# Kernel optimization log

Hardware: AMD Instinct MI355X
Metric: run time of the kernel (lower is better)

## Reference

```python
import jax, jax.numpy as jnp
import numpy as np

B, N, D, H = 8, 1024, 1024, 16
HEAD_DIM = D // H
SCALING = HEAD_DIM ** (-0.5)
NEG = -1000000000.0


def setup_inputs() -> dict:
    key = jax.random.key(0)
    ks = jax.random.split(key, 7)
    x = jax.random.normal(ks[0], (B, N, D), dtype=jnp.float32)
    # variable-length batch: lengths in [N//2, N], mask[b, i] = i < len_b
    lengths = jax.random.randint(ks[1], (B,), N // 2, N + 1)
    mask = jnp.arange(N)[None, :] < lengths[:, None]  # [B, N] bool
    s = D ** (-0.5)
    Wk = jax.random.normal(ks[2], (D, D), dtype=jnp.float32) * s
    Wq = jax.random.normal(ks[3], (D, D), dtype=jnp.float32) * s
    Wv = jax.random.normal(ks[4], (D, D), dtype=jnp.float32) * s
    Wo = jax.random.normal(ks[5], (D, D), dtype=jnp.float32) * s
    bo = jnp.zeros((D,), dtype=jnp.float32)
    return {"x": x, "mask": mask, "Wk": Wk, "Wq": Wq, "Wv": Wv, "Wo": Wo, "bo": bo}


def reference(x, mask, Wk, Wq, Wv, Wo, bo):
    # torch nn.Linear: y = x @ W.T
    keys = (x @ Wk.T).reshape(B, N, H, HEAD_DIM)
    queries = (x @ Wq.T).reshape(B, N, H, HEAD_DIM)
    values = (x @ Wv.T).reshape(B, N, H, HEAD_DIM)
    # NOTE: faithful to source: keys on i, queries on j, softmax over j
    scores = jnp.einsum('bihx,bjhx->bhij', keys, queries) * SCALING  # [B,H,N,N]
    pair_mask = mask[:, None, :] & mask[:, :, None]                  # [B,N,N]
    scores = scores + jnp.where(pair_mask, 0.0, NEG)[:, None, :, :]
    attn = jax.nn.softmax(scores, axis=-1)
    out = jnp.einsum('bhij,bjhx->bihx', attn, values)                # [B,N,H,hd]
    out = out.reshape(B, N, D)
    out = out @ Wo.T + bo
    # source does out_dense[mask] (ragged); static-shape equivalent: zero padding
    return out * mask[:, :, None].astype(out.dtype)
```

## Files before the change

### kernel.cpp

```cpp
#include <hip/hip_runtime.h>

typedef unsigned short u16;
typedef __attribute__((ext_vector_type(8))) short short8;
typedef __attribute__((ext_vector_type(4))) short short4v;
typedef __attribute__((ext_vector_type(4))) float f32x4;
typedef __attribute__((ext_vector_type(16))) float f32x16;

#define MFMA16(a, b, c) __builtin_amdgcn_mfma_f32_16x16x32_bf16(a, b, c, 0, 0, 0)
#define MFMA32(a, b, c) __builtin_amdgcn_mfma_f32_32x32x16_bf16(a, b, c, 0, 0, 0)

#define BB 8
#define NN 1024
#define DD 1024
#define HH 16
#define HD 64
#define MM (BB * NN)
#define SCLOG2 0.18033688011112042f

static __device__ __forceinline__ u16 f2bf(float f) {
  unsigned u = __float_as_uint(f);
  u += 0x7fffu + ((u >> 16) & 1u);
  return (u16)(u >> 16);
}

static __device__ __forceinline__ void gld16(const void* g, void* l) {
  __builtin_amdgcn_global_load_lds((const __attribute__((address_space(1))) void*)g,
                                   (__attribute__((address_space(3))) void*)l, 16, 0, 0);
}

static __device__ __forceinline__ unsigned cvtpk(float lo, float hi) {
  unsigned r;
  asm("v_cvt_pk_bf16_f32 %0, %1, %2" : "=v"(r) : "v"(lo), "v"(hi));
  return r;
}

static __device__ __forceinline__ f32x16 zero16() {
  f32x16 v;
#pragma unroll
  for (int i = 0; i < 16; ++i) v[i] = 0.f;
  return v;
}

__global__ __launch_bounds__(256) void cast_bf16_kernel(const float* __restrict__ in,
                                                        u16* __restrict__ out, int n8) {
  const int i = blockIdx.x * 256 + threadIdx.x;
  if (i >= n8) return;
  const f32x4* p = (const f32x4*)in + (size_t)i * 2;
  const f32x4 a = p[0], b = p[1];
  short8 o;
  o[0] = (short)f2bf(a[0]); o[1] = (short)f2bf(a[1]);
  o[2] = (short)f2bf(a[2]); o[3] = (short)f2bf(a[3]);
  o[4] = (short)f2bf(b[0]); o[5] = (short)f2bf(b[1]);
  o[6] = (short)f2bf(b[2]); o[7] = (short)f2bf(b[3]);
  *(short8*)(out + (size_t)i * 8) = o;
}

__global__ __launch_bounds__(256) void cast4_lens_kernel(const float* __restrict__ a, const float* __restrict__ b,
                                                         const float* __restrict__ c, const float* __restrict__ d,
                                                         u16* __restrict__ oa, u16* __restrict__ ob,
                                                         u16* __restrict__ oc, u16* __restrict__ od,
                                                         const unsigned char* __restrict__ mask,
                                                         int* __restrict__ lens) {
  if (blockIdx.y == 4) {
    if (blockIdx.x != 0) return;
    __shared__ int acc[BB];
    const int t = threadIdx.x;
    if (t < BB) acc[t] = 0;
    __syncthreads();
    const bool isbyte = (mask[1] != 0);
    for (int bb = 0; bb < BB; ++bb) {
      int s = 0;
      if (isbyte) {
        for (int i = t; i < NN; i += 256) s += mask[(size_t)bb * NN + i] ? 1 : 0;
      } else {
        const int* mi = (const int*)mask;
        for (int i = t; i < NN; i += 256) s += mi[(size_t)bb * NN + i] != 0 ? 1 : 0;
      }
      if (s) atomicAdd(&acc[bb], s);
    }
    __syncthreads();
    if (t < BB) lens[t] = acc[t];
    return;
  }
  const int i = blockIdx.x * 256 + threadIdx.x;
  const float* in;
  u16* out;
  switch (blockIdx.y) {
    case 0: in = a; out = oa; break;
    case 1: in = b; out = ob; break;
    case 2: in = c; out = oc; break;
    default: in = d; out = od; break;
  }
  const f32x4* p = (const f32x4*)in + (size_t)i * 2;
  const f32x4 va = p[0], vb = p[1];
  short8 o;
  o[0] = (short)f2bf(va[0]); o[1] = (short)f2bf(va[1]);
  o[2] = (short)f2bf(va[2]); o[3] = (short)f2bf(va[3]);
  o[4] = (short)f2bf(vb[0]); o[5] = (short)f2bf(vb[1]);
  o[6] = (short)f2bf(vb[2]); o[7] = (short)f2bf(vb[3]);
  *(short8*)(out + (size_t)i * 8) = o;
}

#define STAGE_G(d, k0_)                                                            \
  _Pragma("unroll") for (int p = 0; p < 2; ++p) {                                  \
    const int off = (p * 256 + t) * 16;                                            \
    const int row = off >> 6;                                                      \
    const int colb = (off & 63) ^ (((row >> 1) & 3) << 4);                         \
    gld16(Ag + (size_t)(m0 + row) * 1024 + (k0_) + (colb >> 1), &As[d][off >> 1]); \
    gld16(Bg + (size_t)(n0 + row) * 1024 + (k0_) + (colb >> 1), &Bs[d][off >> 1]); \
  }

#define GEMM_CORE2()                                                            \
  STAGE_G(0, 0)                                                                 \
  __syncthreads();                                                              \
  for (int k0 = 0; k0 < 1024; k0 += 32) {                                       \
    const int cur = (k0 >> 5) & 1;                                              \
    if (k0 + 32 < 1024) { STAGE_G(cur ^ 1, k0 + 32) }                           \
    short8 af[4], bf[4];                                                        \
    _Pragma("unroll") for (int mi = 0; mi < 4; ++mi) {                          \
      const int row = wr * 64 + mi * 16 + li;                                   \
      const int byo = row * 64 + ((lg * 16) ^ (((row >> 1) & 3) << 4));         \
      af[mi] = *(const short8*)((const char*)&As[cur][0] + byo);                \
    }                                                                           \
    _Pragma("unroll") for (int ni = 0; ni < 4; ++ni) {                          \
      const int row = wc * 64 + ni * 16 + li;                                   \
      const int byo = row * 64 + ((lg * 16) ^ (((row >> 1) & 3) << 4));         \
      bf[ni] = *(const short8*)((const char*)&Bs[cur][0] + byo);                \
    }                                                                           \
    __builtin_amdgcn_s_setprio(1);                                              \
    _Pragma("unroll") for (int mi = 0; mi < 4; ++mi)                            \
      _Pragma("unroll") for (int ni = 0; ni < 4; ++ni)                          \
          acc[mi][ni] = MFMA16(af[mi], bf[ni], acc[mi][ni]);                    \
    __builtin_amdgcn_s_setprio(0);                                              \
    __syncthreads();                                                            \
  }

__global__ __launch_bounds__(256) void gemm_qkv(const u16* __restrict__ A,
                                                const u16* __restrict__ Wk3, const u16* __restrict__ Wq3,
                                                const u16* __restrict__ Wv3,
                                                u16* __restrict__ kb, u16* __restrict__ qb,
                                                u16* __restrict__ vtb, const int* __restrict__ lens) {
  const int m0 = blockIdx.x * 128;
  if ((m0 & 1023) >= lens[m0 >> 10]) return;
  __shared__ u16 As[2][4096];
  __shared__ u16 Bs[2][4096];
  const int mat = blockIdx.y >> 3;
  const int n0 = (blockIdx.y & 7) * 128;
  const u16* Ag = A;
  const u16* Bg = (mat == 0) ? Wk3 : (mat == 1) ? Wq3 : Wv3;
  const int t = threadIdx.x;
  const int lane = t & 63;
  const int w = t >> 6;
  const int wr = w >> 1, wc = w & 1;
  const int li = lane & 15, lg = lane >> 4;
  f32x4 acc[4][4] = {};

  GEMM_CORE2()

  if (mat == 2) {
#pragma unroll
    for (int mi = 0; mi < 4; ++mi) {
      const int row = m0 + wr * 64 + mi * 16 + lg * 4;
      const int bb = row >> 10, jj = row & 1023;
#pragma unroll
      for (int ni = 0; ni < 4; ++ni) {
        const int col = n0 + wc * 64 + ni * 16 + li;
        const int h = col >> 6, x = col & 63;
        short4v st;
#pragma unroll
        for (int r = 0; r < 4; ++r) st[r] = (short)f2bf(acc[mi][ni][r]);
        *(short4v*)(vtb + ((size_t)((bb * HH + h) * HD + x)) * NN + jj) = st;
      }
    }
  } else {
    u16* C = (mat == 0) ? kb : qb;
    const float scale = (mat == 0) ? SCLOG2 : 1.0f;
#pragma unroll
    for (int mi = 0; mi < 4; ++mi)
#pragma unroll
      for (int ni = 0; ni < 4; ++ni) {
        const int col = n0 + wc * 64 + ni * 16 + li;
        const int rowb = m0 + wr * 64 + mi * 16 + lg * 4;
#pragma unroll
        for (int r = 0; r < 4; ++r)
          C[(size_t)(rowb + r) * 1024 + col] = f2bf(acc[mi][ni][r] * scale);
      }
  }
}

__global__ __launch_bounds__(256) void gemm_out(const u16* __restrict__ A, const u16* __restrict__ Bw,
                                                float* __restrict__ C, const float* __restrict__ bias,
                                                const int* __restrict__ lens) {
  const int m0 = blockIdx.x * 128;
  const int n0 = blockIdx.y * 128;
  const int t = threadIdx.x;
  if ((m0 & 1023) >= lens[m0 >> 10]) {
    const int r = t >> 1, ch = (t & 1) * 64;
    float* Crow = C + (size_t)(m0 + r) * 1024 + n0 + ch;
    const f32x4 z = {0.f, 0.f, 0.f, 0.f};
#pragma unroll
    for (int c = 0; c < 16; ++c) *(f32x4*)(Crow + c * 4) = z;
    return;
  }
  __shared__ u16 As[2][4096];
  __shared__ u16 Bs[2][4096];
  const u16* Ag = A;
  const u16* Bg = Bw;
  const int lane = t & 63;
  const int w = t >> 6;
  const int wr = w >> 1, wc = w & 1;
  const int li = lane & 15, lg = lane >> 4;
  f32x4 acc[4][4] = {};

  GEMM_CORE2()

#pragma unroll
  for (int ni = 0; ni < 4; ++ni) {
    const int col = n0 + wc * 64 + ni * 16 + li;
    const float bv = bias[col];
#pragma unroll
    for (int mi = 0; mi < 4; ++mi) {
      const int rowb = m0 + wr * 64 + mi * 16 + lg * 4;
#pragma unroll
      for (int r = 0; r < 4; ++r) {
        const int row = rowb + r;
        const int bb = row >> 10, ii = row & 1023;
        const float v = (ii < lens[bb]) ? (acc[mi][ni][r] + bv) : 0.f;
        C[(size_t)row * 1024 + col] = v;
      }
    }
  }
}

#define QK_PART(JC, SN0_, SN1_)                                                \
  { const u16* Qc = &Qs[(JC) & 1][0];                                          \
    SN0_ = zero16(); SN1_ = zero16();                                          \
    __builtin_amdgcn_s_setprio(1);                                             \
    _Pragma("unroll") for (int ks = 0; ks < 4; ++ks) {                         \
      const short8 qf = *(const short8*)(Qc + (ks * 64 + l) * 8);              \
      SN0_ = MFMA32(qf, kf[ks], SN0_); }                                       \
    _Pragma("unroll") for (int ks = 0; ks < 4; ++ks) {                         \
      const short8 qf = *(const short8*)(Qc + ((4 + ks) * 64 + l) * 8);        \
      SN1_ = MFMA32(qf, kf[ks], SN1_); }                                       \
    __builtin_amdgcn_s_setprio(0); }

#define V_READ(JC, VF_)                                                        \
  { const u16* Vc = &Vs[(JC) & 1][0];                                          \
    _Pragma("unroll") for (int kk = 0; kk < 8; ++kk)                           \
      VF_[kk] = *(const short8*)(Vc + (kk * 64 + l) * 8); }

#define SM_PV(S0_, S1_, VF_)                                                   \
  {                                                                            \
    float pmax = S0_[0];                                                       \
    _Pragma("unroll") for (int r = 1; r < 16; ++r) pmax = fmaxf(pmax, S0_[r]); \
    _Pragma("unroll") for (int r = 0; r < 16; ++r) pmax = fmaxf(pmax, S1_[r]); \
    pmax = fmaxf(pmax, __shfl_xor(pmax, 32));                                  \
    if (!__all(pmax <= m_run + 11.5f)) {                    \
      const float mnew = fmaxf(m_run, pmax);                                   \
      const float al = __builtin_amdgcn_exp2f(m_run - mnew);                   \
      l_run *= al;                                                             \
      _Pragma("unroll") for (int r = 0; r < 16; ++r) { o0[r] *= al; o1[r] *= al; } \
      m_run = mnew;                                                            \
    }                                                                          \
    float rs = 0.f;                                                            \
    _Pragma("unroll") for (int r = 0; r < 16; ++r) {                           \
      const float p = __builtin_amdgcn_exp2f(S0_[r] - m_run); S0_[r] = p; rs += p; } \
    _Pragma("unroll") for (int r = 0; r < 16; ++r) {                           \
      const float p = __builtin_amdgcn_exp2f(S1_[r] - m_run); S1_[r] = p; rs += p; } \
    rs += __shfl_xor(rs, 32);                                                  \
    l_run += rs;                                                               \
                     \
    short8 pf[4];                                                              \
    _Pragma("unroll") for (int jk = 0; jk < 4; ++jk) {                         \
      const f32x16& ss = (jk < 2) ? S0_ : S1_;                                 \
      const int kk2 = jk & 1;                                                  \
      unsigned W0 = cvtpk(ss[8 * kk2 + 0], ss[8 * kk2 + 1]);                   \
      unsigned W1 = cvtpk(ss[8 * kk2 + 2], ss[8 * kk2 + 3]);                   \
      unsigned W2 = cvtpk(ss[8 * kk2 + 4], ss[8 * kk2 + 5]);                   \
      unsigned W3 = cvtpk(ss[8 * kk2 + 6], ss[8 * kk2 + 7]);                   \
      asm("v_permlane32_swap_b32 %0, %1" : "+v"(W0), "+v"(W2));                \
      asm("v_permlane32_swap_b32 %0, %1" : "+v"(W1), "+v"(W3));                \
      union { unsigned u[4]; short8 s; } pu;                                   \
      pu.u[0] = W0; pu.u[1] = W1; pu.u[2] = W2; pu.u[3] = W3;                  \
      pf[jk] = pu.s;                                                           \
    }                                                                          \
    __builtin_amdgcn_s_setprio(1);                                             \
    _Pragma("unroll") for (int kg = 0; kg < 4; ++kg) o0 = MFMA32(VF_[kg], pf[kg], o0); \
    _Pragma("unroll") for (int kg = 0; kg < 4; ++kg) o1 = MFMA32(VF_[4 + kg], pf[kg], o1); \
    __builtin_amdgcn_s_setprio(0);                                             \
  }

#define MASK_LAST(S0_, S1_)                                                    \
  { const int j0m = (nt - 1) * 64;                                             \
    if (j0m + 64 > len) {                                                      \
      _Pragma("unroll") for (int r = 0; r < 16; ++r) {                         \
        const int jl = (r & 3) + 8 * (r >> 2) + 4 * hi;                        \
        if (j0m + jl >= len) S0_[r] = -3.0e38f;                                \
        if (j0m + 32 + jl >= len) S1_[r] = -3.0e38f;                           \
      } } }

#define ATTN_BODY(JT, SP0, SP1, VFP, SN0, SN1, VFN)                            \
  { const int jc = (JT);                                                       \
    if (jc + 1 < nt) STAGE((jc + 1) & 1, (jc + 1) * 64);                       \
    QK_PART(jc, SN0, SN1)                                                      \
    SM_PV(SP0, SP1, VFP)                                                       \
    V_READ(jc, VFN)                                                            \
    __syncthreads(); }

__global__ __launch_bounds__(256) void attn_kernel(const u16* __restrict__ Kb, const u16* __restrict__ Qb,
                                                   const u16* __restrict__ Vtb, u16* __restrict__ attb,
                                                   const int* __restrict__ lens) {
  const int bid = blockIdx.x;
  const int b = bid >> 7;
  const int ic = (bid >> 3) & 7;
  const int h = ((bid & 7) << 1) | ((bid >> 6) & 1);
  const int len = lens[b];
  const int i0 = ic * 128;
  if (i0 >= len) return;
  const int t = threadIdx.x;
  const int w = t >> 6, l = t & 63;
  const int l31 = l & 31, hi = l >> 5;
  const int i0w = i0 + w * 32;

  __shared__ u16 Qs[2][4096];
  __shared__ u16 Vs[2][4096];

  short8 kf[4];
  {
    const u16* kp = Kb + ((size_t)(b * NN + i0w + l31)) * DD + h * HD + hi * 8;
#pragma unroll
    for (int ks = 0; ks < 4; ++ks) kf[ks] = *(const short8*)(kp + ks * 16);
  }

  const size_t qsrc = ((size_t)(b * NN) + l31) * DD + h * HD + w * 16 + hi * 8;
  const size_t vsrc = ((size_t)((b * HH + h) * HD + l31)) * NN + w * 16 + hi * 8;

  auto STAGE = [&](int buf, int j0) {
    u16* qd = &Qs[buf][0] + t * 8;
    u16* vd = &Vs[buf][0] + t * 8;
    gld16(Qb + qsrc + (size_t)j0 * DD, qd);
    gld16(Qb + qsrc + (size_t)(j0 + 32) * DD, qd + 2048);
    gld16(Vtb + vsrc + j0, vd);
    gld16(Vtb + vsrc + 32 * NN + j0, vd + 2048);
  };

  f32x16 o0 = zero16(), o1 = zero16();
  float m_run = -3.0e38f, l_run = 0.f;
  const int nt = (len + 63) >> 6;

  f32x16 sA0, sA1, sB0, sB1;
  short8 vfA[8], vfB[8];

  STAGE(0, 0);
  __syncthreads();
  if (nt > 1) STAGE(1, 64);
  QK_PART(0, sA0, sA1)
  V_READ(0, vfA)
  __syncthreads();

  int jt = 1;
  for (; jt + 1 < nt; jt += 2) {
    ATTN_BODY(jt, sA0, sA1, vfA, sB0, sB1, vfB)
    ATTN_BODY(jt + 1, sB0, sB1, vfB, sA0, sA1, vfA)
  }
  if (jt < nt) {
    ATTN_BODY(jt, sA0, sA1, vfA, sB0, sB1, vfB)
    MASK_LAST(sB0, sB1)
    SM_PV(sB0, sB1, vfB)
  } else {
    MASK_LAST(sA0, sA1)
    SM_PV(sA0, sA1, vfA)
  }

  const float inv = 1.f / l_run;
  u16* op = attb + (size_t)(b * NN + i0w + l31) * DD + h * HD + hi * 4;
#pragma unroll
  for (int xs = 0; xs < 2; ++xs) {
    const f32x16& oo = xs ? o1 : o0;
#pragma unroll
    for (int q = 0; q < 4; ++q) {
      short4v st;
#pragma unroll
      for (int e = 0; e < 4; ++e) st[e] = (short)f2bf(oo[q * 4 + e] * inv);
      *(short4v*)(op + xs * 32 + q * 8) = st;
    }
  }
}

extern "C" void kernel_launch(void* const* d_in, const int* in_sizes, int n_in,
                              void* d_out, int out_size, void* d_ws, size_t ws_size,
                              hipStream_t stream) {
  const float* x = (const float*)d_in[0];
  const unsigned char* mask = (const unsigned char*)d_in[1];
  const float* Wk = (const float*)d_in[2];
  const float* Wq = (const float*)d_in[3];
  const float* Wv = (const float*)d_in[4];
  const float* Wo = (const float*)d_in[5];
  const float* bo = (const float*)d_in[6];
  float* out = (float*)d_out;

  char* ws = (char*)d_ws;
  size_t o = 0;
  int* lens = (int*)(ws + o); o += 256;
  u16* xb  = (u16*)(ws + o); o += (size_t)MM * DD * 2;
  u16* wkb = (u16*)(ws + o); o += (size_t)DD * DD * 2;
  u16* wqb = (u16*)(ws + o); o += (size_t)DD * DD * 2;
  u16* wvb = (u16*)(ws + o); o += (size_t)DD * DD * 2;
  u16* wob = (u16*)(ws + o); o += (size_t)DD * DD * 2;
  u16* kb  = (u16*)(ws + o); o += (size_t)MM * DD * 2;
  u16* qb  = (u16*)(ws + o); o += (size_t)MM * DD * 2;
  u16* vtb = (u16*)(ws + o); o += (size_t)MM * DD * 2;
  u16* attb = xb;

  const int xn8 = MM * DD / 8;
  cast_bf16_kernel<<<dim3(xn8 / 256), dim3(256), 0, stream>>>(x, xb, xn8);
  cast4_lens_kernel<<<dim3(DD * DD / 8 / 256, 5), dim3(256), 0, stream>>>(
      Wk, Wq, Wv, Wo, wkb, wqb, wvb, wob, mask, lens);

  gemm_qkv<<<dim3(MM / 128, 24), dim3(256), 0, stream>>>(xb, wkb, wqb, wvb, kb, qb, vtb, lens);

  attn_kernel<<<dim3(1024), dim3(256), 0, stream>>>(kb, qb, vtb, attb, lens);

  gemm_out<<<dim3(MM / 128, DD / 128), dim3(256), 0, stream>>>(attb, wob, out, bo, lens);
}
```

Measured before the change: 180.5 us.

## Triple-buffer GEMM LDS staging with explicit vmcnt waits and split barriers

```diff
diff --git a/kernel.cpp b/kernel.cpp
--- a/kernel.cpp
+++ b/kernel.cpp
@@ -16,6 +16,8 @@
 #define HD 64
 #define MM (BB * NN)
 #define SCLOG2 0.18033688011112042f
+
+#define WAIT_VM(N) asm volatile("s_waitcnt vmcnt(" #N ")" ::: "memory")
 
 static __device__ __forceinline__ u16 f2bf(float f) {
   unsigned u = __float_as_uint(f);
@@ -101,7 +103,7 @@
   *(short8*)(out + (size_t)i * 8) = o;
 }
 
-#define STAGE_G(d, k0_)                                                            \
+#define STAGE_B(d, k0_)                                                            \
   _Pragma("unroll") for (int p = 0; p < 2; ++p) {                                  \
     const int off = (p * 256 + t) * 16;                                            \
     const int row = off >> 6;                                                      \
@@ -110,29 +112,40 @@
     gld16(Bg + (size_t)(n0 + row) * 1024 + (k0_) + (colb >> 1), &Bs[d][off >> 1]); \
   }
 
-#define GEMM_CORE2()                                                            \
-  STAGE_G(0, 0)                                                                 \
-  __syncthreads();                                                              \
-  for (int k0 = 0; k0 < 1024; k0 += 32) {                                       \
-    const int cur = (k0 >> 5) & 1;                                              \
-    if (k0 + 32 < 1024) { STAGE_G(cur ^ 1, k0 + 32) }                           \
+#define GEMM_CORE4()                                                            \
+  STAGE_B(0, 0)                                                                 \
+  STAGE_B(1, 32)                                                                \
+  _Pragma("unroll") for (int kt = 0; kt < 32; ++kt) {                           \
+    asm volatile("" ::: "memory");                                              \
+    __builtin_amdgcn_s_barrier();                                    \
+    if (kt < 30) {                                                              \
+      const int bn = (kt + 2) % 3;                                              \
+      STAGE_B(bn, (kt + 2) * 32)                                                \
+      WAIT_VM(8);                                                               \
+    } else if (kt == 30) {                                                      \
+      WAIT_VM(4);                                                               \
+    } else {                                                                    \
+      WAIT_VM(0);                                                               \
+    }                                                                           \
+    __builtin_amdgcn_s_barrier();                                    \
+    asm volatile("" ::: "memory");                                              \
+    const int bc = kt % 3;                                                      \
     short8 af[4], bf[4];                                                        \
     _Pragma("unroll") for (int mi = 0; mi < 4; ++mi) {                          \
       const int row = wr * 64 + mi * 16 + li;                                   \
       const int byo = row * 64 + ((lg * 16) ^ (((row >> 1) & 3) << 4));         \
-      af[mi] = *(const short8*)((const char*)&As[cur][0] + byo);                \
+      af[mi] = *(const short8*)((const char*)&As[bc][0] + byo);                 \
     }                                                                           \
     _Pragma("unroll") for (int ni = 0; ni < 4; ++ni) {                          \
       const int row = wc * 64 + ni * 16 + li;                                   \
       const int byo = row * 64 + ((lg * 16) ^ (((row >> 1) & 3) << 4));         \
-      bf[ni] = *(const short8*)((const char*)&Bs[cur][0] + byo);                \
+      bf[ni] = *(const short8*)((const char*)&Bs[bc][0] + byo);                 \
     }                                                                           \
     __builtin_amdgcn_s_setprio(1);                                              \
     _Pragma("unroll") for (int mi = 0; mi < 4; ++mi)                            \
       _Pragma("unroll") for (int ni = 0; ni < 4; ++ni)                          \
           acc[mi][ni] = MFMA16(af[mi], bf[ni], acc[mi][ni]);                    \
     __builtin_amdgcn_s_setprio(0);                                              \
-    __syncthreads();                                                            \
   }
 
 __global__ __launch_bounds__(256) void gemm_qkv(const u16* __restrict__ A,
@@ -142,8 +155,8 @@
                                                 u16* __restrict__ vtb, const int* __restrict__ lens) {
   const int m0 = blockIdx.x * 128;
   if ((m0 & 1023) >= lens[m0 >> 10]) return;
-  __shared__ u16 As[2][4096];
-  __shared__ u16 Bs[2][4096];
+  __shared__ u16 As[3][4096];
+  __shared__ u16 Bs[3][4096];
   const int mat = blockIdx.y >> 3;
   const int n0 = (blockIdx.y & 7) * 128;
   const u16* Ag = A;
@@ -155,7 +168,7 @@
   const int li = lane & 15, lg = lane >> 4;
   f32x4 acc[4][4] = {};
 
-  GEMM_CORE2()
+  GEMM_CORE4()
 
   if (mat == 2) {
 #pragma unroll
@@ -202,8 +215,8 @@
     for (int c = 0; c < 16; ++c) *(f32x4*)(Crow + c * 4) = z;
     return;
   }
-  __shared__ u16 As[2][4096];
-  __shared__ u16 Bs[2][4096];
+  __shared__ u16 As[3][4096];
+  __shared__ u16 Bs[3][4096];
   const u16* Ag = A;
   const u16* Bg = Bw;
   const int lane = t & 63;
@@ -212,7 +225,7 @@
   const int li = lane & 15, lg = lane >> 4;
   f32x4 acc[4][4] = {};
 
-  GEMM_CORE2()
+  GEMM_CORE4()
 
 #pragma unroll
   for (int ni = 0; ni < 4; ++ni) {
@@ -269,7 +282,6 @@
       const float p = __builtin_amdgcn_exp2f(S1_[r] - m_run); S1_[r] = p; rs += p; } \
     rs += __shfl_xor(rs, 32);                                                  \
     l_run += rs;                                                               \
-                     \
     short8 pf[4];                                                              \
     _Pragma("unroll") for (int jk = 0; jk < 4; ++jk) {                         \
       const f32x16& ss = (jk < 2) ? S0_ : S1_;                                 \
```

Result: no change. 179.9 us (-0.3%).
